# Optimization experiments

Hardware: AMD Instinct MI355X
Metric: run time of the kernel (lower is better)

Reference implementation:

```python
import jax, jax.numpy as jnp
import numpy as np

B, T, H, OUT_STEPS, D = 131072, 51, 64, 20, 4


def setup_inputs() -> dict:
    key = jax.random.key(0)
    ks = jax.random.split(key, 11)
    s = 1.0 / np.sqrt(H)  # torch nn.GRU / nn.Linear uniform init bound
    u = lambda k, shape: jax.random.uniform(k, shape, jnp.float32, -s, s)
    return {
        "input_seq": jax.random.normal(ks[0], (B, T, D), jnp.float32),
        "enc_Wih": u(ks[1], (3 * H, D)),
        "enc_Whh": u(ks[2], (3 * H, H)),
        "enc_bih": u(ks[3], (3 * H,)),
        "enc_bhh": u(ks[4], (3 * H,)),
        "dec_Wih": u(ks[5], (3 * H, D)),
        "dec_Whh": u(ks[6], (3 * H, H)),
        "dec_bih": u(ks[7], (3 * H,)),
        "dec_bhh": u(ks[8], (3 * H,)),
        "lin_W": u(ks[9], (D, H)),
        "lin_b": u(ks[10], (D,)),
    }


def _gru_cell(x, h, Wih, Whh, bih, bhh):
    """PyTorch GRU cell semantics. x: [B,D_in], h: [B,H]."""
    gi = x @ Wih.T + bih  # [B,3H]
    gh = h @ Whh.T + bhh  # [B,3H]
    ir, iz, inn = jnp.split(gi, 3, axis=-1)
    hr, hz, hn = jnp.split(gh, 3, axis=-1)
    r = jax.nn.sigmoid(ir + hr)
    z = jax.nn.sigmoid(iz + hz)
    n = jnp.tanh(inn + r * hn)
    return (1.0 - z) * n + z * h


def reference(input_seq, enc_Wih, enc_Whh, enc_bih, enc_bhh,
              dec_Wih, dec_Whh, dec_bih, dec_bhh, lin_W, lin_b):
    # offset: last observed point, broadcast over the 20 output steps
    offset = input_seq[:, -1:, :]  # [B,1,D]
    diffs = input_seq[:, 1:] - input_seq[:, :-1]  # [B,T-1,D]; dropout p=0 -> identity
    h0 = jnp.zeros((input_seq.shape[0], H), input_seq.dtype)

    def enc_step(h, x_t):
        return _gru_cell(x_t, h, enc_Wih, enc_Whh, enc_bih, enc_bhh), None

    hn, _ = jax.lax.scan(enc_step, h0, jnp.swapaxes(diffs, 0, 1))  # final hidden [B,H]

    def dec_step(carry, _):
        h, px = carry
        h = _gru_cell(px, h, dec_Wih, dec_Whh, dec_bih, dec_bhh)
        x = h @ lin_W.T + lin_b + px  # linear + residual
        return (h, x), x

    _, xs = jax.lax.scan(dec_step, (hn, diffs[:, -1]), None, length=OUT_STEPS)
    out = jnp.swapaxes(xs, 0, 1)  # [B,OUT_STEPS,D]
    return out + offset
```

## Files before the change

kernel.cpp:

```cpp
#include <hip/hip_runtime.h>
#include <hip/hip_bf16.h>

namespace {

constexpr int kT = 51;
constexpr int kOut = 20;
constexpr float kL2E  = 1.4426950408889634f;
constexpr float kL2E2 = 2.8853900817779268f;

typedef __attribute__((ext_vector_type(8))) short bf16x8;
typedef __attribute__((ext_vector_type(4))) float f32x4;

union FragU {
    bf16x8 v;
    unsigned long long u64[2];
    unsigned int u32[4];
    unsigned short s[8];
};

__device__ __forceinline__ unsigned short f2bf(float x) {
    union { float f; unsigned int u; } v;
    v.f = x;
    unsigned int r = (v.u + 0x7fffu + ((v.u >> 16) & 1u)) >> 16;
    return (unsigned short)r;
}

__device__ __forceinline__ unsigned int packbf(float a, float b) {
    union { float f; unsigned int u; } ua, ub;
    ua.f = a; ub.f = b;
    return __builtin_amdgcn_perm(ub.u + 0x8000u, ua.u + 0x8000u, 0x07060302u);
}

__global__ __launch_bounds__(256, 4) void gru_encdec(
    const float* __restrict__ input,
    const float* __restrict__ eWih, const float* __restrict__ eWhh,
    const float* __restrict__ ebih, const float* __restrict__ ebhh,
    const float* __restrict__ dWih, const float* __restrict__ dWhh,
    const float* __restrict__ dbih, const float* __restrict__ dbhh,
    const float* __restrict__ linW, const float* __restrict__ linb,
    float* __restrict__ out)
{
    __shared__ __align__(16) unsigned short hbuf[2][16 * 68];
    __shared__ __align__(16) float sout[16 * 84];

    const int lane = (int)(threadIdx.x & 63u);
    const int w = (int)(threadIdx.x >> 6u);
    const int q = lane >> 4;
    const int i = lane & 15;
    const long b = (long)blockIdx.x * 16 + i;
    const float* __restrict__ xrow = input + b * (kT * 4);
    const bool q0 = (q == 0);

    bf16x8 WA[3][2];
    bf16x8 WAUG[3];
    f32x4 bhhn4;
    float hprev[4];
    bf16x8 bh0 = {0, 0, 0, 0, 0, 0, 0, 0};
    bf16x8 bh1 = {0, 0, 0, 0, 0, 0, 0, 0};
    float px[4];
    const f32x4 z4 = {0.f, 0.f, 0.f, 0.f};
    int sel = 0;

    auto load_whh = [&](const float* __restrict__ Whh) {
#pragma unroll
        for (int l = 0; l < 3; ++l) {
            const int tau = 4 * l + w;
            const float sc = (l < 2) ? kL2E : kL2E2;
#pragma unroll
            for (int f = 0; f < 2; ++f) {
                const float* ptr = Whh + (tau * 16 + i) * 64 + f * 32 + q * 8;
                FragU fu;
#pragma unroll
                for (int j = 0; j < 8; ++j) fu.s[j] = f2bf(ptr[j] * sc);
                WA[l][f] = fu.v;
            }
        }
    };

    auto load_aug = [&](const float* __restrict__ Wih,
                        const float* __restrict__ bih,
                        const float* __restrict__ bhh) {
#pragma unroll
        for (int l = 0; l < 3; ++l) {
            const int tau = 4 * l + w;
            const float sc = (l < 2) ? kL2E : kL2E2;
            FragU fu;
            fu.u64[0] = 0; fu.u64[1] = 0;
            if (q0) {
                int j = tau * 16 + i;
#pragma unroll
                for (int d = 0; d < 4; ++d) fu.s[d] = f2bf(Wih[j * 4 + d] * sc);
                float bias = (l < 2) ? (bih[j] + bhh[j]) : bih[j];
                fu.s[4] = f2bf(bias * sc);
            }
            WAUG[l] = fu.v;
        }
#pragma unroll
        for (int r = 0; r < 4; ++r)
            bhhn4[r] = bhh[128 + 16 * w + 4 * q + r] * kL2E2;
    };

    auto make_baug = [&]() -> bf16x8 {
        FragU fu;
        unsigned int p01 = packbf(px[0], px[1]);
        unsigned int p23 = packbf(px[2], px[3]);
        fu.u32[0] = q0 ? p01 : 0u;
        fu.u32[1] = q0 ? p23 : 0u;
        fu.u32[2] = q0 ? 0x3f80u : 0u;
        fu.u32[3] = 0u;
        return fu.v;
    };

    auto gru_step = [&](bf16x8 baug) {
        unsigned short* __restrict__ hw = hbuf[sel];
        f32x4 accR = __builtin_amdgcn_mfma_f32_16x16x32_bf16(WAUG[0], baug, z4, 0, 0, 0);
        accR = __builtin_amdgcn_mfma_f32_16x16x32_bf16(WA[0][0], bh0, accR, 0, 0, 0);
        accR = __builtin_amdgcn_mfma_f32_16x16x32_bf16(WA[0][1], bh1, accR, 0, 0, 0);
        f32x4 accZ = __builtin_amdgcn_mfma_f32_16x16x32_bf16(WAUG[1], baug, z4, 0, 0, 0);
        accZ = __builtin_amdgcn_mfma_f32_16x16x32_bf16(WA[1][0], bh0, accZ, 0, 0, 0);
        accZ = __builtin_amdgcn_mfma_f32_16x16x32_bf16(WA[1][1], bh1, accZ, 0, 0, 0);
        f32x4 accNi = __builtin_amdgcn_mfma_f32_16x16x32_bf16(WAUG[2], baug, z4, 0, 0, 0);
        f32x4 accNh = __builtin_amdgcn_mfma_f32_16x16x32_bf16(WA[2][0], bh0, bhhn4, 0, 0, 0);
        accNh = __builtin_amdgcn_mfma_f32_16x16x32_bf16(WA[2][1], bh1, accNh, 0, 0, 0);

        float hv[4];
#pragma unroll
        for (int r = 0; r < 4; ++r) {
            float a = __builtin_amdgcn_exp2f(-accR[r]);
            float bb = __builtin_amdgcn_exp2f(-accZ[r]);
            float A = 1.f + a;
            float Bv = 1.f + bb;
            float rp = __builtin_amdgcn_rcpf(A * Bv);
            float rr = rp * Bv;
            float zz = rp * A;
            float pre2 = __builtin_fmaf(rr, accNh[r], accNi[r]);
            float tt = __builtin_amdgcn_rcpf(__builtin_amdgcn_exp2f(pre2) + 1.f);
            float nn = __builtin_fmaf(-2.f, tt, 1.f);
            float hp = hprev[r];
            hv[r] = __builtin_fmaf(zz, hp - nn, nn);
            hprev[r] = hv[r];
        }
        uint2 wv;
        wv.x = packbf(hv[0], hv[1]);
        wv.y = packbf(hv[2], hv[3]);
        *(uint2*)&hw[i * 68 + 16 * w + 4 * q] = wv;

        __syncthreads();
        FragU f0, f1;
        f0.u64[0] = *(const unsigned long long*)&hw[i * 68 + 8 * q];
        f0.u64[1] = *(const unsigned long long*)&hw[i * 68 + 8 * q + 4];
        f1.u64[0] = *(const unsigned long long*)&hw[i * 68 + 32 + 8 * q];
        f1.u64[1] = *(const unsigned long long*)&hw[i * 68 + 32 + 8 * q + 4];
        bh0 = f0.v;
        bh1 = f1.v;
        sel ^= 1;
    };

#pragma unroll
    for (int r = 0; r < 4; ++r) hprev[r] = 0.f;
    load_whh(eWhh);
    load_aug(eWih, ebih, ebhh);

    float4 xp = *(const float4*)(xrow);
    float4 xn = *(const float4*)(xrow + 4);
#pragma unroll 1
    for (int s = 0; s < kT - 1; ++s) {
        int idx = s + 2; if (idx > kT - 1) idx = kT - 1;
        float4 xf = *(const float4*)(xrow + idx * 4);
        px[0] = xn.x - xp.x;
        px[1] = xn.y - xp.y;
        px[2] = xn.z - xp.z;
        px[3] = xn.w - xp.w;
        gru_step(make_baug());
        xp = xn;
        xn = xf;
    }
    float4 offv = xp;

    load_whh(dWhh);
    load_aug(dWih, dbih, dbhh);

    bf16x8 AL0, AL1, AL2;
    {
        FragU a0, a1, a2;
        a0.u64[0] = a0.u64[1] = 0;
        a1.u64[0] = a1.u64[1] = 0;
        a2.u64[0] = a2.u64[1] = 0;
        if (i < 4) {
            const float* p0 = linW + i * 64 + q * 8;
            const float* p1 = linW + i * 64 + 32 + q * 8;
#pragma unroll
            for (int j = 0; j < 8; ++j) {
                a0.s[j] = f2bf(p0[j]);
                a1.s[j] = f2bf(p1[j]);
            }
            if (q0) a2.s[4] = f2bf(linb[i]);
        }
        AL0 = a0.v; AL1 = a1.v; AL2 = a2.v;
    }

#pragma unroll 1
    for (int s = 0; s < kOut; ++s) {
        bf16x8 baug = make_baug();
        gru_step(baug);
        f32x4 accX = __builtin_amdgcn_mfma_f32_16x16x32_bf16(AL2, baug, z4, 0, 0, 0);
        accX = __builtin_amdgcn_mfma_f32_16x16x32_bf16(AL0, bh0, accX, 0, 0, 0);
        accX = __builtin_amdgcn_mfma_f32_16x16x32_bf16(AL1, bh1, accX, 0, 0, 0);
        float x0 = accX[0] + px[0];
        float x1 = accX[1] + px[1];
        float x2 = accX[2] + px[2];
        float x3 = accX[3] + px[3];
        if (w == 0 && q0) {
            float* sr = sout + i * 84 + s * 4;
            sr[0] = x0 + offv.x;
            sr[1] = x1 + offv.y;
            sr[2] = x2 + offv.z;
            sr[3] = x3 + offv.w;
        }
        px[0] = x0; px[1] = x1; px[2] = x2; px[3] = x3;
    }

    if (w == 0) {
        float* __restrict__ go = out + (long)blockIdx.x * 16 * (kOut * 4);
#pragma unroll
        for (int it = 0; it < 5; ++it) {
            int g = it * 256 + lane * 4;
            int row = g / 80;
            int e = g - row * 80;
            float4 v = *(const float4*)&sout[row * 84 + e];
            *(float4*)&go[g] = v;
        }
    }
}

}

extern "C" void kernel_launch(void* const* d_in, const int* in_sizes, int n_in,
                              void* d_out, int out_size, void* d_ws, size_t ws_size,
                              hipStream_t stream) {
    const float* input = (const float*)d_in[0];
    const float* eWih = (const float*)d_in[1];
    const float* eWhh = (const float*)d_in[2];
    const float* ebih = (const float*)d_in[3];
    const float* ebhh = (const float*)d_in[4];
    const float* dWih = (const float*)d_in[5];
    const float* dWhh = (const float*)d_in[6];
    const float* dbih = (const float*)d_in[7];
    const float* dbhh = (const float*)d_in[8];
    const float* linW = (const float*)d_in[9];
    const float* linb = (const float*)d_in[10];
    float* out = (float*)d_out;

    const int B = in_sizes[0] / (kT * 4);
    const int nblocks = B / 16;
    gru_encdec<<<nblocks, 256, 0, stream>>>(input, eWih, eWhh, ebih, ebhh,
                                            dWih, dWhh, dbih, dbhh,
                                            linW, linb, out);
}
```

Baseline: 691.8 us.

## Process two 16-row batch tiles per block to amortize barriers and weights

Each block now handles 32 batch rows as two independent 16-row tiles that share the register-resident weight fragments. The MFMA chains of the two tiles are interleaved, so one tile's dependent latency is hidden by the other. Each __syncthreads per step now serves both tiles, and the reciprocals in the gate math are shared through a product trick. This raises register pressure, so launch bounds drop to 3 blocks per CU, and make_baug now writes x data into non-q0 lanes, relying on the zero-padded weight fragments to cancel those terms.

New measurement: 659.0 us. 4.7% less time.

```diff
diff --git a/kernel.cpp b/kernel.cpp
--- a/kernel.cpp
+++ b/kernel.cpp
@@ -31,7 +31,7 @@
     return __builtin_amdgcn_perm(ub.u + 0x8000u, ua.u + 0x8000u, 0x07060302u);
 }
 
-__global__ __launch_bounds__(256, 4) void gru_encdec(
+__global__ __launch_bounds__(256, 3) void gru_encdec(
     const float* __restrict__ input,
     const float* __restrict__ eWih, const float* __restrict__ eWhh,
     const float* __restrict__ ebih, const float* __restrict__ ebhh,
@@ -40,26 +40,26 @@
     const float* __restrict__ linW, const float* __restrict__ linb,
     float* __restrict__ out)
 {
-    __shared__ __align__(16) unsigned short hbuf[2][16 * 68];
-    __shared__ __align__(16) float sout[16 * 84];
+    __shared__ __align__(16) unsigned short hbuf[2][2][16 * 68];
+    __shared__ __align__(16) float sout[2][16 * 84];
 
     const int lane = (int)(threadIdx.x & 63u);
     const int w = (int)(threadIdx.x >> 6u);
     const int q = lane >> 4;
     const int i = lane & 15;
-    const long b = (long)blockIdx.x * 16 + i;
-    const float* __restrict__ xrow = input + b * (kT * 4);
+    const long b0 = (long)blockIdx.x * 32 + i;
+    const float* __restrict__ xrow0 = input + b0 * (kT * 4);
+    const float* __restrict__ xrow1 = xrow0 + 16 * (kT * 4);
     const bool q0 = (q == 0);
 
     bf16x8 WA[3][2];
     bf16x8 WAUG[3];
     f32x4 bhhn4;
-    float hprev[4];
-    bf16x8 bh0 = {0, 0, 0, 0, 0, 0, 0, 0};
-    bf16x8 bh1 = {0, 0, 0, 0, 0, 0, 0, 0};
-    float px[4];
+    float hp0[4], hp1[4];
+    bf16x8 bhA0 = {0,0,0,0,0,0,0,0}, bhB0 = {0,0,0,0,0,0,0,0};
+    bf16x8 bhA1 = {0,0,0,0,0,0,0,0}, bhB1 = {0,0,0,0,0,0,0,0};
+    float px0[4], px1[4];
     const f32x4 z4 = {0.f, 0.f, 0.f, 0.f};
-    int sel = 0;
 
     auto load_whh = [&](const float* __restrict__ Whh) {
 #pragma unroll
@@ -100,82 +100,108 @@
             bhhn4[r] = bhh[128 + 16 * w + 4 * q + r] * kL2E2;
     };
 
-    auto make_baug = [&]() -> bf16x8 {
+    auto make_baug = [&](const float* px) -> bf16x8 {
         FragU fu;
-        unsigned int p01 = packbf(px[0], px[1]);
-        unsigned int p23 = packbf(px[2], px[3]);
-        fu.u32[0] = q0 ? p01 : 0u;
-        fu.u32[1] = q0 ? p23 : 0u;
-        fu.u32[2] = q0 ? 0x3f80u : 0u;
+        fu.u32[0] = packbf(px[0], px[1]);
+        fu.u32[1] = packbf(px[2], px[3]);
+        fu.u32[2] = 0x3f80u;
         fu.u32[3] = 0u;
         return fu.v;
     };
 
-    auto gru_step = [&](bf16x8 baug) {
-        unsigned short* __restrict__ hw = hbuf[sel];
-        f32x4 accR = __builtin_amdgcn_mfma_f32_16x16x32_bf16(WAUG[0], baug, z4, 0, 0, 0);
-        accR = __builtin_amdgcn_mfma_f32_16x16x32_bf16(WA[0][0], bh0, accR, 0, 0, 0);
-        accR = __builtin_amdgcn_mfma_f32_16x16x32_bf16(WA[0][1], bh1, accR, 0, 0, 0);
-        f32x4 accZ = __builtin_amdgcn_mfma_f32_16x16x32_bf16(WAUG[1], baug, z4, 0, 0, 0);
-        accZ = __builtin_amdgcn_mfma_f32_16x16x32_bf16(WA[1][0], bh0, accZ, 0, 0, 0);
-        accZ = __builtin_amdgcn_mfma_f32_16x16x32_bf16(WA[1][1], bh1, accZ, 0, 0, 0);
-        f32x4 accNi = __builtin_amdgcn_mfma_f32_16x16x32_bf16(WAUG[2], baug, z4, 0, 0, 0);
-        f32x4 accNh = __builtin_amdgcn_mfma_f32_16x16x32_bf16(WA[2][0], bh0, bhhn4, 0, 0, 0);
-        accNh = __builtin_amdgcn_mfma_f32_16x16x32_bf16(WA[2][1], bh1, accNh, 0, 0, 0);
-
-        float hv[4];
+    auto gru_step2 = [&](int ssel, bf16x8 ba0, bf16x8 ba1) {
+        unsigned short* __restrict__ hw0 = hbuf[ssel][0];
+        unsigned short* __restrict__ hw1 = hbuf[ssel][1];
+        f32x4 R0 = __builtin_amdgcn_mfma_f32_16x16x32_bf16(WAUG[0], ba0, z4, 0, 0, 0);
+        R0 = __builtin_amdgcn_mfma_f32_16x16x32_bf16(WA[0][0], bhA0, R0, 0, 0, 0);
+        R0 = __builtin_amdgcn_mfma_f32_16x16x32_bf16(WA[0][1], bhB0, R0, 0, 0, 0);
+        f32x4 Z0 = __builtin_amdgcn_mfma_f32_16x16x32_bf16(WAUG[1], ba0, z4, 0, 0, 0);
+        Z0 = __builtin_amdgcn_mfma_f32_16x16x32_bf16(WA[1][0], bhA0, Z0, 0, 0, 0);
+        Z0 = __builtin_amdgcn_mfma_f32_16x16x32_bf16(WA[1][1], bhB0, Z0, 0, 0, 0);
+        f32x4 Ni0 = __builtin_amdgcn_mfma_f32_16x16x32_bf16(WAUG[2], ba0, z4, 0, 0, 0);
+        f32x4 Nh0 = __builtin_amdgcn_mfma_f32_16x16x32_bf16(WA[2][0], bhA0, bhhn4, 0, 0, 0);
+        Nh0 = __builtin_amdgcn_mfma_f32_16x16x32_bf16(WA[2][1], bhB0, Nh0, 0, 0, 0);
+        f32x4 R1 = __builtin_amdgcn_mfma_f32_16x16x32_bf16(WAUG[0], ba1, z4, 0, 0, 0);
+        R1 = __builtin_amdgcn_mfma_f32_16x16x32_bf16(WA[0][0], bhA1, R1, 0, 0, 0);
+        R1 = __builtin_amdgcn_mfma_f32_16x16x32_bf16(WA[0][1], bhB1, R1, 0, 0, 0);
+        f32x4 Z1 = __builtin_amdgcn_mfma_f32_16x16x32_bf16(WAUG[1], ba1, z4, 0, 0, 0);
+        Z1 = __builtin_amdgcn_mfma_f32_16x16x32_bf16(WA[1][0], bhA1, Z1, 0, 0, 0);
+        Z1 = __builtin_amdgcn_mfma_f32_16x16x32_bf16(WA[1][1], bhB1, Z1, 0, 0, 0);
+        f32x4 Ni1 = __builtin_amdgcn_mfma_f32_16x16x32_bf16(WAUG[2], ba1, z4, 0, 0, 0);
+        f32x4 Nh1 = __builtin_amdgcn_mfma_f32_16x16x32_bf16(WA[2][0], bhA1, bhhn4, 0, 0, 0);
+        Nh1 = __builtin_amdgcn_mfma_f32_16x16x32_bf16(WA[2][1], bhB1, Nh1, 0, 0, 0);
+
+        float hv0[4], hv1[4];
 #pragma unroll
         for (int r = 0; r < 4; ++r) {
-            float a = __builtin_amdgcn_exp2f(-accR[r]);
-            float bb = __builtin_amdgcn_exp2f(-accZ[r]);
-            float A = 1.f + a;
-            float Bv = 1.f + bb;
-            float rp = __builtin_amdgcn_rcpf(A * Bv);
-            float rr = rp * Bv;
-            float zz = rp * A;
-            float pre2 = __builtin_fmaf(rr, accNh[r], accNi[r]);
-            float tt = __builtin_amdgcn_rcpf(__builtin_amdgcn_exp2f(pre2) + 1.f);
-            float nn = __builtin_fmaf(-2.f, tt, 1.f);
-            float hp = hprev[r];
-            hv[r] = __builtin_fmaf(zz, hp - nn, nn);
-            hprev[r] = hv[r];
-        }
-        uint2 wv;
-        wv.x = packbf(hv[0], hv[1]);
-        wv.y = packbf(hv[2], hv[3]);
-        *(uint2*)&hw[i * 68 + 16 * w + 4 * q] = wv;
+            float a0 = __builtin_amdgcn_exp2f(-R0[r]);
+            float c0 = __builtin_amdgcn_exp2f(-Z0[r]);
+            float a1 = __builtin_amdgcn_exp2f(-R1[r]);
+            float c1 = __builtin_amdgcn_exp2f(-Z1[r]);
+            float A0 = 1.f + a0, C0 = 1.f + c0, P0 = A0 * C0;
+            float A1 = 1.f + a1, C1 = 1.f + c1, P1 = A1 * C1;
+            float rpp = __builtin_amdgcn_rcpf(P0 * P1);
+            float rp0 = rpp * P1, rp1 = rpp * P0;
+            float rr0 = rp0 * C0, zz0 = rp0 * A0;
+            float rr1 = rp1 * C1, zz1 = rp1 * A1;
+            float p20 = __builtin_fmaf(rr0, Nh0[r], Ni0[r]);
+            float p21 = __builtin_fmaf(rr1, Nh1[r], Ni1[r]);
+            float E0 = __builtin_amdgcn_exp2f(p20);
+            float E1 = __builtin_amdgcn_exp2f(p21);
+            float D0 = E0 + 1.f, D1 = E1 + 1.f;
+            float rdd = __builtin_amdgcn_rcpf(D0 * D1);
+            float t0 = rdd * D1, t1 = rdd * D0;
+            float n0 = __builtin_fmaf(-2.f, t0, 1.f);
+            float n1 = __builtin_fmaf(-2.f, t1, 1.f);
+            hv0[r] = __builtin_fmaf(zz0, hp0[r] - n0, n0);
+            hv1[r] = __builtin_fmaf(zz1, hp1[r] - n1, n1);
+            hp0[r] = hv0[r];
+            hp1[r] = hv1[r];
+        }
+        uint2 wv0, wv1;
+        wv0.x = packbf(hv0[0], hv0[1]); wv0.y = packbf(hv0[2], hv0[3]);
+        wv1.x = packbf(hv1[0], hv1[1]); wv1.y = packbf(hv1[2], hv1[3]);
+        *(uint2*)&hw0[i * 68 + 16 * w + 4 * q] = wv0;
+        *(uint2*)&hw1[i * 68 + 16 * w + 4 * q] = wv1;
 
         __syncthreads();
-        FragU f0, f1;
-        f0.u64[0] = *(const unsigned long long*)&hw[i * 68 + 8 * q];
-        f0.u64[1] = *(const unsigned long long*)&hw[i * 68 + 8 * q + 4];
-        f1.u64[0] = *(const unsigned long long*)&hw[i * 68 + 32 + 8 * q];
-        f1.u64[1] = *(const unsigned long long*)&hw[i * 68 + 32 + 8 * q + 4];
-        bh0 = f0.v;
-        bh1 = f1.v;
-        sel ^= 1;
-    };
-
-#pragma unroll
-    for (int r = 0; r < 4; ++r) hprev[r] = 0.f;
+        FragU f0, f1, g0f, g1f;
+        f0.u64[0]  = *(const unsigned long long*)&hw0[i * 68 + 8 * q];
+        f0.u64[1]  = *(const unsigned long long*)&hw0[i * 68 + 8 * q + 4];
+        f1.u64[0]  = *(const unsigned long long*)&hw0[i * 68 + 32 + 8 * q];
+        f1.u64[1]  = *(const unsigned long long*)&hw0[i * 68 + 32 + 8 * q + 4];
+        g0f.u64[0] = *(const unsigned long long*)&hw1[i * 68 + 8 * q];
+        g0f.u64[1] = *(const unsigned long long*)&hw1[i * 68 + 8 * q + 4];
+        g1f.u64[0] = *(const unsigned long long*)&hw1[i * 68 + 32 + 8 * q];
+        g1f.u64[1] = *(const unsigned long long*)&hw1[i * 68 + 32 + 8 * q + 4];
+        bhA0 = f0.v;  bhB0 = f1.v;
+        bhA1 = g0f.v; bhB1 = g1f.v;
+    };
+
+#pragma unroll
+    for (int r = 0; r < 4; ++r) { hp0[r] = 0.f; hp1[r] = 0.f; }
     load_whh(eWhh);
     load_aug(eWih, ebih, ebhh);
 
-    float4 xp = *(const float4*)(xrow);
-    float4 xn = *(const float4*)(xrow + 4);
-#pragma unroll 1
+    float4 xp0 = *(const float4*)(xrow0);
+    float4 xn0 = *(const float4*)(xrow0 + 4);
+    float4 xp1 = *(const float4*)(xrow1);
+    float4 xn1 = *(const float4*)(xrow1 + 4);
+#pragma unroll 2
     for (int s = 0; s < kT - 1; ++s) {
         int idx = s + 2; if (idx > kT - 1) idx = kT - 1;
-        float4 xf = *(const float4*)(xrow + idx * 4);
-        px[0] = xn.x - xp.x;
-        px[1] = xn.y - xp.y;
-        px[2] = xn.z - xp.z;
-        px[3] = xn.w - xp.w;
-        gru_step(make_baug());
-        xp = xn;
-        xn = xf;
-    }
-    float4 offv = xp;
+        float4 xf0 = *(const float4*)(xrow0 + idx * 4);
+        float4 xf1 = *(const float4*)(xrow1 + idx * 4);
+        px0[0] = xn0.x - xp0.x; px0[1] = xn0.y - xp0.y;
+        px0[2] = xn0.z - xp0.z; px0[3] = xn0.w - xp0.w;
+        px1[0] = xn1.x - xp1.x; px1[1] = xn1.y - xp1.y;
+        px1[2] = xn1.z - xp1.z; px1[3] = xn1.w - xp1.w;
+        gru_step2(s & 1, make_baug(px0), make_baug(px1));
+        xp0 = xn0; xn0 = xf0;
+        xp1 = xn1; xn1 = xf1;
+    }
+    float4 off0 = xp0;
+    float4 off1 = xp1;
 
     load_whh(dWhh);
     load_aug(dWih, dbih, dbhh);
@@ -199,35 +225,40 @@
         AL0 = a0.v; AL1 = a1.v; AL2 = a2.v;
     }
 
-#pragma unroll 1
+#pragma unroll 2
     for (int s = 0; s < kOut; ++s) {
-        bf16x8 baug = make_baug();
-        gru_step(baug);
-        f32x4 accX = __builtin_amdgcn_mfma_f32_16x16x32_bf16(AL2, baug, z4, 0, 0, 0);
-        accX = __builtin_amdgcn_mfma_f32_16x16x32_bf16(AL0, bh0, accX, 0, 0, 0);
-        accX = __builtin_amdgcn_mfma_f32_16x16x32_bf16(AL1, bh1, accX, 0, 0, 0);
-        float x0 = accX[0] + px[0];
-        float x1 = accX[1] + px[1];
-        float x2 = accX[2] + px[2];
-        float x3 = accX[3] + px[3];
+        bf16x8 ba0 = make_baug(px0);
+        bf16x8 ba1 = make_baug(px1);
+        gru_step2(s & 1, ba0, ba1);
+        f32x4 X0 = __builtin_amdgcn_mfma_f32_16x16x32_bf16(AL2, ba0, z4, 0, 0, 0);
+        X0 = __builtin_amdgcn_mfma_f32_16x16x32_bf16(AL0, bhA0, X0, 0, 0, 0);
+        X0 = __builtin_amdgcn_mfma_f32_16x16x32_bf16(AL1, bhB0, X0, 0, 0, 0);
+        f32x4 X1 = __builtin_amdgcn_mfma_f32_16x16x32_bf16(AL2, ba1, z4, 0, 0, 0);
+        X1 = __builtin_amdgcn_mfma_f32_16x16x32_bf16(AL0, bhA1, X1, 0, 0, 0);
+        X1 = __builtin_amdgcn_mfma_f32_16x16x32_bf16(AL1, bhB1, X1, 0, 0, 0);
+        px0[0] += X0[0]; px0[1] += X0[1]; px0[2] += X0[2]; px0[3] += X0[3];
+        px1[0] += X1[0]; px1[1] += X1[1]; px1[2] += X1[2]; px1[3] += X1[3];
         if (w == 0 && q0) {
-            float* sr = sout + i * 84 + s * 4;
-            sr[0] = x0 + offv.x;
-            sr[1] = x1 + offv.y;
-            sr[2] = x2 + offv.z;
-            sr[3] = x3 + offv.w;
-        }
-        px[0] = x0; px[1] = x1; px[2] = x2; px[3] = x3;
-    }
-
-    if (w == 0) {
-        float* __restrict__ go = out + (long)blockIdx.x * 16 * (kOut * 4);
+            float* sr = sout[0] + i * 84 + s * 4;
+            sr[0] = px0[0] + off0.x; sr[1] = px0[1] + off0.y;
+            sr[2] = px0[2] + off0.z; sr[3] = px0[3] + off0.w;
+        }
+        if (w == 1 && q0) {
+            float* sr = sout[1] + i * 84 + s * 4;
+            sr[0] = px1[0] + off1.x; sr[1] = px1[1] + off1.y;
+            sr[2] = px1[2] + off1.z; sr[3] = px1[3] + off1.w;
+        }
+    }
+
+    if (w < 2) {
+        float* __restrict__ go = out + ((long)blockIdx.x * 32 + w * 16) * (kOut * 4);
+        const float* __restrict__ so = sout[w];
 #pragma unroll
         for (int it = 0; it < 5; ++it) {
             int g = it * 256 + lane * 4;
             int row = g / 80;
             int e = g - row * 80;
-            float4 v = *(const float4*)&sout[row * 84 + e];
+            float4 v = *(const float4*)&so[row * 84 + e];
             *(float4*)&go[g] = v;
         }
     }
@@ -252,7 +283,7 @@
     float* out = (float*)d_out;
 
     const int B = in_sizes[0] / (kT * 4);
-    const int nblocks = B / 16;
+    const int nblocks = B / 32;
     gru_encdec<<<nblocks, 256, 0, stream>>>(input, eWih, eWhh, ebih, ebhh,
                                             dWih, dWhh, dbih, dbhh,
                                             linW, linb, out);
```
